# Kernel tuning notes

Measured on AMD Instinct MI355X. Metric: run time of the kernel, lower is better.

The kernel has to match this reference:

```python
import jax, jax.numpy as jnp
import numpy as np

NUM_HEADS = 12


def setup_inputs() -> dict:
    key = jax.random.key(0)
    ks = jax.random.split(key, 8)
    B, H, W, C = 1, 64, 64, 768
    hd = C // NUM_HEADS
    s = 0.02
    return {
        "hidden_states": jax.random.normal(ks[0], (B, H, W, C), jnp.float32),
        "q_w": jax.random.normal(ks[1], (C, C), jnp.float32) * s,
        "q_b": jnp.zeros((C,), jnp.float32),
        "k_w": jax.random.normal(ks[2], (C, C), jnp.float32) * s,
        "k_b": jnp.zeros((C,), jnp.float32),
        "v_w": jax.random.normal(ks[3], (C, C), jnp.float32) * s,
        "v_b": jnp.zeros((C,), jnp.float32),
        "proj_w": jax.random.normal(ks[4], (C, C), jnp.float32) * s,
        "proj_b": jnp.zeros((C,), jnp.float32),
        "rel_pos_h": jax.random.normal(ks[5], (2 * H - 1, hd), jnp.float32) * s,
        "rel_pos_w": jax.random.normal(ks[6], (2 * W - 1, hd), jnp.float32) * s,
    }


def reference(hidden_states, q_w, q_b, k_w, k_b, v_w, v_b, proj_w, proj_b,
              rel_pos_h, rel_pos_w):
    B, H, W, C = hidden_states.shape
    nh = NUM_HEADS
    hd = C // nh
    scale = hd ** -0.5

    x = hidden_states.reshape(B, H * W, C)

    def to_heads(t):  # [B, HW, C] -> [B*nh, HW, hd]
        return t.reshape(B, H * W, nh, hd).transpose(0, 2, 1, 3).reshape(B * nh, H * W, hd)

    q = to_heads(x @ q_w.T + q_b)
    k = to_heads(x @ k_w.T + k_b)
    v = to_heads(x @ v_w.T + v_b)

    # scaled QK^T: [B*nh, HW, HW]
    attn = jnp.einsum("bqd,bkd->bqk", q * scale, k)

    # decomposed relative position bias (q_size == k_size, so no interpolation)
    idx_h = jnp.arange(H)[:, None] - jnp.arange(H)[None, :] + (H - 1)
    idx_w = jnp.arange(W)[:, None] - jnp.arange(W)[None, :] + (W - 1)
    Rh = rel_pos_h[idx_h]  # [H, H, hd]
    Rw = rel_pos_w[idx_w]  # [W, W, hd]
    r_q = q.reshape(B * nh, H, W, hd)
    rel_h = jnp.einsum("bhwc,hkc->bhwk", r_q, Rh)  # [B*nh, H, W, H]
    rel_w = jnp.einsum("bhwc,wkc->bhwk", r_q, Rw)  # [B*nh, H, W, W]
    attn = (attn.reshape(B * nh, H, W, H, W)
            + rel_h[:, :, :, :, None]
            + rel_w[:, :, :, None, :]).reshape(B * nh, H * W, H * W)

    attn = jax.nn.softmax(attn.astype(jnp.float32), axis=-1).astype(q.dtype)
    # dropout p=0.0 in eval -> identity

    out = jnp.einsum("bqk,bkd->bqd", attn, v)
    out = out.reshape(B, nh, H, W, hd).transpose(0, 2, 3, 1, 4).reshape(B, H, W, C)
    out = out @ proj_w.T + proj_b
    return out
```

## Files before the change

### kernel.cpp

```cpp
#include <hip/hip_runtime.h>
#include <cstdint>
#include <cstddef>

#define T 4096
#define C 768
#define HD 64
#define NH 12

typedef float f32x4 __attribute__((ext_vector_type(4)));
typedef __bf16 bf16x8 __attribute__((ext_vector_type(8)));
typedef short s16x4 __attribute__((ext_vector_type(4)));
typedef unsigned short u16;

static __device__ __forceinline__ u16 f2bf(float f) {
    union { __bf16 h; u16 u; } cv;
    cv.h = (__bf16)f;
    return cv.u;
}

static __device__ __forceinline__ float exp2_hw(float x) {
    float r;
    asm("v_exp_f32 %0, %1" : "=v"(r) : "v"(x));
    return r;
}

static __device__ __forceinline__ void load_lds16(const void* g, void* l) {
    __builtin_amdgcn_global_load_lds(
        (const __attribute__((address_space(1))) void*)g,
        (__attribute__((address_space(3))) void*)l, 16, 0, 0);
}

static __device__ __forceinline__ void mfma16(f32x4& acc, s16x4 a, s16x4 b) {
#if defined(__HIP_DEVICE_COMPILE__)
#if __has_builtin(__builtin_amdgcn_mfma_f32_16x16x16bf16_1k)
    acc = __builtin_amdgcn_mfma_f32_16x16x16bf16_1k(a, b, acc, 0, 0, 0);
#else
    asm volatile("s_nop 2\n\t"
                 "v_mfma_f32_16x16x16_bf16 %0, %1, %2, %0\n\t"
                 "s_nop 7\n\t"
                 "s_nop 7"
                 : "+v"(acc) : "v"(a), "v"(b));
#endif
#else
    (void)acc; (void)a; (void)b;
#endif
}

__global__ __launch_bounds__(256) void cvt_main(
    const float* __restrict__ hs, const float* __restrict__ w0,
    const float* __restrict__ w1, const float* __restrict__ w2,
    const float* __restrict__ w3,
    u16* __restrict__ dhs, u16* __restrict__ dw0, u16* __restrict__ dw1,
    u16* __restrict__ dw2, u16* __restrict__ dw3) {
    const int NHS = T * C;
    const int NW = C * C;
    int i = (blockIdx.x * 256 + threadIdx.x) * 4;
    const float* s; u16* d; int j;
    if (i < NHS) { s = hs; d = dhs; j = i; }
    else {
        j = i - NHS;
        int t = j / NW; j -= t * NW;
        s = (t == 0) ? w0 : (t == 1) ? w1 : (t == 2) ? w2 : w3;
        d = (t == 0) ? dw0 : (t == 1) ? dw1 : (t == 2) ? dw2 : dw3;
    }
    float4 v = *(const float4*)(s + j);
    d[j + 0] = f2bf(v.x);
    d[j + 1] = f2bf(v.y);
    d[j + 2] = f2bf(v.z);
    d[j + 3] = f2bf(v.w);
}

__global__ __launch_bounds__(256) void cvt_rel(const float* __restrict__ rh,
                                               const float* __restrict__ rw,
                                               u16* __restrict__ drh,
                                               u16* __restrict__ drw) {
    const int N = 127 * HD;
    int i = (blockIdx.x * 256 + threadIdx.x) * 4;
    if (i >= 2 * N) return;
    const float* s = (i < N) ? rh : rw;
    u16* d = (i < N) ? drh : drw;
    int j = (i < N) ? i : i - N;
    float4 v = *(const float4*)(s + j);
    d[j + 0] = f2bf(v.x);
    d[j + 1] = f2bf(v.y);
    d[j + 2] = f2bf(v.z);
    d[j + 3] = f2bf(v.w);
}

__global__ __launch_bounds__(256, 2) void gemm_qkv_kernel(
    const u16* __restrict__ xb,
    const u16* __restrict__ wq, const u16* __restrict__ wk, const u16* __restrict__ wv,
    const float* __restrict__ qb, const float* __restrict__ kb, const float* __restrict__ vb,
    u16* __restrict__ Q, u16* __restrict__ K, u16* __restrict__ V) {
    __shared__ __align__(16) u16 As[2][128 * 64];
    __shared__ __align__(16) u16 Bs[2][128 * 64];
    const int z = blockIdx.z;
    const u16* W = (z == 0) ? wq : (z == 1) ? wk : wv;
    const float* bias = (z == 0) ? qb : (z == 1) ? kb : vb;
    u16* dst = (z == 0) ? Q : (z == 1) ? K : V;
    const int m0 = blockIdx.x * 128, n0 = blockIdx.y * 128;
    const int tid = threadIdx.x;
    const int wave = tid >> 6, lane = tid & 63, quad = lane >> 4, l15 = lane & 15;
    const int r0 = (wave >> 1) * 64, c0 = (wave & 1) * 64;
    int srow[4], sx[4], sdst[4];
#pragma unroll
    for (int i = 0; i < 4; ++i) {
        int p = i * 256 + wave * 64 + lane;
        srow[i] = p >> 3;
        sx[i] = (p & 7) ^ (srow[i] & 7);
        sdst[i] = (i * 256 + wave * 64) * 8;
    }
    f32x4 acc[4][4] = {};
#pragma unroll
    for (int i = 0; i < 4; ++i) {
        load_lds16(xb + (size_t)(m0 + srow[i]) * C + sx[i] * 8, &As[0][sdst[i]]);
        load_lds16(W + (size_t)(n0 + srow[i]) * C + sx[i] * 8, &Bs[0][sdst[i]]);
    }
    for (int kt = 0; kt < 12; ++kt) {
        const int cur = kt & 1;
        __syncthreads();
        if (kt < 11) {
            const int k0 = (kt + 1) * 64;
#pragma unroll
            for (int i = 0; i < 4; ++i) {
                load_lds16(xb + (size_t)(m0 + srow[i]) * C + k0 + sx[i] * 8, &As[cur ^ 1][sdst[i]]);
                load_lds16(W + (size_t)(n0 + srow[i]) * C + k0 + sx[i] * 8, &Bs[cur ^ 1][sdst[i]]);
            }
        }
#pragma unroll
        for (int kk = 0; kk < 2; ++kk) {
            bf16x8 af[4], bfr[4];
#pragma unroll
            for (int mi = 0; mi < 4; ++mi) {
                int r = r0 + mi * 16 + l15;
                af[mi] = *(const bf16x8*)&As[cur][r * 64 + (((kk * 4 + quad) ^ (r & 7)) * 8)];
            }
#pragma unroll
            for (int ni = 0; ni < 4; ++ni) {
                int r = c0 + ni * 16 + l15;
                bfr[ni] = *(const bf16x8*)&Bs[cur][r * 64 + (((kk * 4 + quad) ^ (r & 7)) * 8)];
            }
#pragma unroll
            for (int mi = 0; mi < 4; ++mi)
#pragma unroll
                for (int ni = 0; ni < 4; ++ni)
                    acc[mi][ni] = __builtin_amdgcn_mfma_f32_16x16x32_bf16(af[mi], bfr[ni], acc[mi][ni], 0, 0, 0);
        }
    }
#pragma unroll
    for (int mi = 0; mi < 4; ++mi)
#pragma unroll
        for (int ni = 0; ni < 4; ++ni)
#pragma unroll
            for (int r = 0; r < 4; ++r) {
                int m = m0 + r0 + mi * 16 + quad * 4 + r;
                int n = n0 + c0 + ni * 16 + l15;
                float v = acc[mi][ni][r] + bias[n];
                dst[(size_t)(n >> 6) * T * HD + (size_t)m * HD + (n & 63)] = f2bf(v);
            }
}

__global__ __launch_bounds__(256, 2) void gemm_proj_kernel(
    const u16* __restrict__ A, const u16* __restrict__ W,
    const float* __restrict__ bias, float* __restrict__ out) {
    __shared__ __align__(16) u16 As[2][128 * 64];
    __shared__ __align__(16) u16 Bs[2][128 * 64];
    const int m0 = blockIdx.x * 128, n0 = blockIdx.y * 128;
    const int tid = threadIdx.x;
    const int wave = tid >> 6, lane = tid & 63, quad = lane >> 4, l15 = lane & 15;
    const int r0 = (wave >> 1) * 64, c0 = (wave & 1) * 64;
    int srow[4], sx[4], sdst[4];
#pragma unroll
    for (int i = 0; i < 4; ++i) {
        int p = i * 256 + wave * 64 + lane;
        srow[i] = p >> 3;
        sx[i] = (p & 7) ^ (srow[i] & 7);
        sdst[i] = (i * 256 + wave * 64) * 8;
    }
    f32x4 acc[4][4] = {};
#pragma unroll
    for (int i = 0; i < 4; ++i) {
        load_lds16(A + (size_t)(m0 + srow[i]) * C + sx[i] * 8, &As[0][sdst[i]]);
        load_lds16(W + (size_t)(n0 + srow[i]) * C + sx[i] * 8, &Bs[0][sdst[i]]);
    }
    for (int kt = 0; kt < 12; ++kt) {
        const int cur = kt & 1;
        __syncthreads();
        if (kt < 11) {
            const int k0 = (kt + 1) * 64;
#pragma unroll
            for (int i = 0; i < 4; ++i) {
                load_lds16(A + (size_t)(m0 + srow[i]) * C + k0 + sx[i] * 8, &As[cur ^ 1][sdst[i]]);
                load_lds16(W + (size_t)(n0 + srow[i]) * C + k0 + sx[i] * 8, &Bs[cur ^ 1][sdst[i]]);
            }
        }
#pragma unroll
        for (int kk = 0; kk < 2; ++kk) {
            bf16x8 af[4], bfr[4];
#pragma unroll
            for (int mi = 0; mi < 4; ++mi) {
                int r = r0 + mi * 16 + l15;
                af[mi] = *(const bf16x8*)&As[cur][r * 64 + (((kk * 4 + quad) ^ (r & 7)) * 8)];
            }
#pragma unroll
            for (int ni = 0; ni < 4; ++ni) {
                int r = c0 + ni * 16 + l15;
                bfr[ni] = *(const bf16x8*)&Bs[cur][r * 64 + (((kk * 4 + quad) ^ (r & 7)) * 8)];
            }
#pragma unroll
            for (int mi = 0; mi < 4; ++mi)
#pragma unroll
                for (int ni = 0; ni < 4; ++ni)
                    acc[mi][ni] = __builtin_amdgcn_mfma_f32_16x16x32_bf16(af[mi], bfr[ni], acc[mi][ni], 0, 0, 0);
        }
    }
#pragma unroll
    for (int mi = 0; mi < 4; ++mi)
#pragma unroll
        for (int ni = 0; ni < 4; ++ni)
#pragma unroll
            for (int r = 0; r < 4; ++r) {
                int m = m0 + r0 + mi * 16 + quad * 4 + r;
                int n = n0 + c0 + ni * 16 + l15;
                out[(size_t)m * C + n] = acc[mi][ni][r] + bias[n];
            }
}

__global__ __launch_bounds__(256) void vtrans_kernel(const u16* __restrict__ V,
                                                     u16* __restrict__ Vt) {
    __shared__ __align__(16) u16 tl[64 * 72];
    const int h = blockIdx.y, t0 = blockIdx.x * 64, tid = threadIdx.x;
#pragma unroll
    for (int i = 0; i < 2; ++i) {
        int c = i * 256 + tid;
        int row = c >> 3, col = (c & 7) * 8;
        union { float4 f; u16 u[8]; } cv;
        cv.f = *(const float4*)(V + (size_t)h * T * HD + (size_t)(t0 + row) * HD + col);
#pragma unroll
        for (int j = 0; j < 8; ++j) tl[(col + j) * 72 + row] = cv.u[j];
    }
    __syncthreads();
#pragma unroll
    for (int i = 0; i < 2; ++i) {
        int c = i * 256 + tid;
        int drow = c >> 3, tcol = (c & 7) * 8;
        float4 v = *(const float4*)&tl[drow * 72 + tcol];
        *(float4*)(Vt + (size_t)(h * HD + drow) * T + t0 + tcol) = v;
    }
}

__global__ __launch_bounds__(256) void relh_kernel(const u16* __restrict__ Q,
                                                   const u16* __restrict__ rph,
                                                   float* __restrict__ relH) {
    const float LOG2E = 1.4426950408889634f;
    const int hq = blockIdx.x, h = blockIdx.y;
    const int tid = threadIdx.x, wave = tid >> 6, lane = tid & 63;
    const int quad = lane >> 4, l15 = lane & 15;
    f32x4 acc[4] = {};
    bf16x8 a[2], b[4][2];
#pragma unroll
    for (int kk = 0; kk < 2; ++kk) {
        int hk = wave * 16 + l15;
        a[kk] = *(const bf16x8*)(rph + (size_t)(hq - hk + 63) * HD + kk * 32 + quad * 8);
    }
#pragma unroll
    for (int nt = 0; nt < 4; ++nt)
#pragma unroll
        for (int kk = 0; kk < 2; ++kk)
            b[nt][kk] = *(const bf16x8*)(Q + (size_t)h * T * HD +
                                         (size_t)(hq * 64 + nt * 16 + l15) * HD + kk * 32 + quad * 8);
#pragma unroll
    for (int nt = 0; nt < 4; ++nt) {
        acc[nt] = __builtin_amdgcn_mfma_f32_16x16x32_bf16(a[0], b[nt][0], acc[nt], 0, 0, 0);
        acc[nt] = __builtin_amdgcn_mfma_f32_16x16x32_bf16(a[1], b[nt][1], acc[nt], 0, 0, 0);
    }
#pragma unroll
    for (int nt = 0; nt < 4; ++nt) {
        float4 v;
        v.x = acc[nt][0] * LOG2E; v.y = acc[nt][1] * LOG2E;
        v.z = acc[nt][2] * LOG2E; v.w = acc[nt][3] * LOG2E;
        *(float4*)(relH + (((size_t)(h * 64 + hq) * 64 + nt * 16 + l15) * 64) +
                   wave * 16 + quad * 4) = v;
    }
}

__global__ __launch_bounds__(256) void relw_kernel(const u16* __restrict__ Q,
                                                   const u16* __restrict__ rpw,
                                                   float* __restrict__ relW) {
    const float LOG2E = 1.4426950408889634f;
    const int wq = blockIdx.x, h = blockIdx.y;
    const int tid = threadIdx.x, wave = tid >> 6, lane = tid & 63;
    const int quad = lane >> 4, l15 = lane & 15;
    f32x4 acc[4] = {};
    bf16x8 a[2], b[4][2];
#pragma unroll
    for (int kk = 0; kk < 2; ++kk) {
        int hqr = wave * 16 + l15;
        a[kk] = *(const bf16x8*)(Q + (size_t)h * T * HD +
                                 (size_t)(hqr * 64 + wq) * HD + kk * 32 + quad * 8);
    }
#pragma unroll
    for (int nt = 0; nt < 4; ++nt)
#pragma unroll
        for (int kk = 0; kk < 2; ++kk) {
            int wk = nt * 16 + l15;
            b[nt][kk] = *(const bf16x8*)(rpw + (size_t)(wq - wk + 63) * HD + kk * 32 + quad * 8);
        }
#pragma unroll
    for (int nt = 0; nt < 4; ++nt) {
        acc[nt] = __builtin_amdgcn_mfma_f32_16x16x32_bf16(a[0], b[nt][0], acc[nt], 0, 0, 0);
        acc[nt] = __builtin_amdgcn_mfma_f32_16x16x32_bf16(a[1], b[nt][1], acc[nt], 0, 0, 0);
    }
#pragma unroll
    for (int nt = 0; nt < 4; ++nt)
#pragma unroll
        for (int r = 0; r < 4; ++r) {
            int hqr = wave * 16 + quad * 4 + r;
            relW[((size_t)h * T + hqr * 64 + wq) * 64 + nt * 16 + l15] = acc[nt][r] * LOG2E;
        }
}

__global__ __launch_bounds__(256, 3) void attn_kernel(
    const u16* __restrict__ Q, const u16* __restrict__ K, const u16* __restrict__ Vt,
    const float* __restrict__ relH, const float* __restrict__ relW,
    u16* __restrict__ AO) {
    __shared__ __align__(16) u16 kbuf[2][64 * 64];
    __shared__ __align__(16) u16 vbuf[2][64 * 64];
    const int hq = blockIdx.x, h = blockIdx.y;
    const int t0 = hq * 64;
    const int tid = threadIdx.x, wave = tid >> 6, lane = tid & 63;
    const int quad = lane >> 4, l15 = lane & 15;
    const float C1 = 0.18033688011112042f;

    const u16* Kbase = K + (size_t)h * T * HD;
    const u16* Vbase = Vt + (size_t)h * HD * T;

    const int p0 = wave * 128 + lane, p1 = p0 + 64;
    const int sr0 = p0 >> 3, sx0 = (p0 & 7) ^ (sr0 & 7);
    const int sr1 = p1 >> 3, sx1 = (p1 & 7) ^ (sr1 & 7);
    const int lds0 = wave * 1024, lds1 = wave * 1024 + 512;

    bf16x8 qa[2];
#pragma unroll
    for (int kk = 0; kk < 2; ++kk)
        qa[kk] = *(const bf16x8*)(Q + (size_t)h * T * HD +
                                  (size_t)(t0 + wave * 16 + l15) * HD + kk * 32 + quad * 8);
    const float* rwb = relW + ((size_t)h * T + (t0 + wave * 16 + l15)) * 64;
    float4 rw4[4];
#pragma unroll
    for (int g = 0; g < 4; ++g)
        rw4[g] = *(const float4*)(rwb + g * 16 + quad * 4);
    const float* rhb = relH + ((size_t)(h * 64 + hq) * 64 + wave * 16 + l15) * 64;

    s16x4 ones;
#pragma unroll
    for (int j = 0; j < 4; ++j) ones[j] = (short)0x3F80;

    f32x4 oa[4] = {};
    f32x4 lacc = {};

    load_lds16(Kbase + sr0 * HD + sx0 * 8, &kbuf[0][lds0]);
    load_lds16(Kbase + sr1 * HD + sx1 * 8, &kbuf[0][lds1]);
    load_lds16(Vbase + (size_t)sr0 * T + sx0 * 8, &vbuf[0][lds0]);
    load_lds16(Vbase + (size_t)sr1 * T + sx1 * 8, &vbuf[0][lds1]);

    for (int hk4 = 0; hk4 < 16; ++hk4) {
        float4 rh4 = *(const float4*)(rhb + hk4 * 4);
#pragma unroll
        for (int rr = 0; rr < 4; ++rr) {
            const int hk = hk4 * 4 + rr;
            const int cur = rr & 1;
            __syncthreads();
            if (hk < 63) {
                const int tk0 = (hk + 1) * 64;
                load_lds16(Kbase + (size_t)(tk0 + sr0) * HD + sx0 * 8, &kbuf[cur ^ 1][lds0]);
                load_lds16(Kbase + (size_t)(tk0 + sr1) * HD + sx1 * 8, &kbuf[cur ^ 1][lds1]);
                load_lds16(Vbase + (size_t)sr0 * T + tk0 + sx0 * 8, &vbuf[cur ^ 1][lds0]);
                load_lds16(Vbase + (size_t)sr1 * T + tk0 + sx1 * 8, &vbuf[cur ^ 1][lds1]);
            }
            const u16* kc = kbuf[cur];
            const u16* vc = vbuf[cur];
            f32x4 s4[4] = {};
#pragma unroll
            for (int g = 0; g < 4; ++g)
#pragma unroll
                for (int kk = 0; kk < 2; ++kk) {
                    bf16x8 af = *(const bf16x8*)&kc[g * 1024 + l15 * 64 +
                                                    (((kk * 4 + quad) ^ (l15 & 7)) * 8)];
                    s4[g] = __builtin_amdgcn_mfma_f32_16x16x32_bf16(af, qa[kk], s4[g], 0, 0, 0);
                }
            const float rhc = (rr == 0) ? rh4.x : (rr == 1) ? rh4.y : (rr == 2) ? rh4.z : rh4.w;
            s16x4 pB[4];
#pragma unroll
            for (int g = 0; g < 4; ++g) {
#pragma unroll
                for (int r = 0; r < 4; ++r) {
                    float e = exp2_hw(s4[g][r] * C1 + (rhc + rw4[g][r]));
                    pB[g][r] = (short)f2bf(e);
                }
            }
#pragma unroll
            for (int g = 0; g < 4; ++g) {
                mfma16(lacc, ones, pB[g]);
#pragma unroll
                for (int dg = 0; dg < 4; ++dg) {
                    s16x4 vf = *(const s16x4*)&vc[dg * 1024 + l15 * 64 +
                                                  (((2 * g + (quad >> 1)) ^ (l15 & 7)) * 8) +
                                                  (quad & 1) * 4];
                    mfma16(oa[dg], vf, pB[g]);
                }
            }
        }
    }
    const float inv = 1.0f / lacc[0];
    const size_t trow = (size_t)(t0 + wave * 16 + l15) * C + h * HD;
#pragma unroll
    for (int dg = 0; dg < 4; ++dg) {
        unsigned int lo = (unsigned int)f2bf(oa[dg][0] * inv) |
                          ((unsigned int)f2bf(oa[dg][1] * inv) << 16);
        unsigned int hi = (unsigned int)f2bf(oa[dg][2] * inv) |
                          ((unsigned int)f2bf(oa[dg][3] * inv) << 16);
        uint2 st; st.x = lo; st.y = hi;
        *(uint2*)(AO + trow + dg * 16 + quad * 4) = st;
    }
}

extern "C" void kernel_launch(void* const* d_in, const int* in_sizes, int n_in,
                              void* d_out, int out_size, void* d_ws, size_t ws_size,
                              hipStream_t stream) {
    (void)in_sizes; (void)n_in; (void)out_size; (void)ws_size;
    const float* hs  = (const float*)d_in[0];
    const float* q_w = (const float*)d_in[1];
    const float* q_b = (const float*)d_in[2];
    const float* k_w = (const float*)d_in[3];
    const float* k_b = (const float*)d_in[4];
    const float* v_w = (const float*)d_in[5];
    const float* v_b = (const float*)d_in[6];
    const float* p_w = (const float*)d_in[7];
    const float* p_b = (const float*)d_in[8];
    const float* rph = (const float*)d_in[9];
    const float* rpw = (const float*)d_in[10];

    char* ws = (char*)d_ws;
    size_t off = 0;
    auto alloc = [&](size_t bytes) {
        void* p = ws + off;
        off = (off + bytes + 255) & ~(size_t)255;
        return p;
    };
    u16* xb   = (u16*)alloc((size_t)T * C * 2);
    u16* wqb  = (u16*)alloc((size_t)C * C * 2);
    u16* wkb  = (u16*)alloc((size_t)C * C * 2);
    u16* wvb  = (u16*)alloc((size_t)C * C * 2);
    u16* wpb  = (u16*)alloc((size_t)C * C * 2);
    u16* rphb = (u16*)alloc((size_t)127 * HD * 2);
    u16* rpwb = (u16*)alloc((size_t)127 * HD * 2);
    u16* Qb   = (u16*)alloc((size_t)NH * T * HD * 2);
    u16* Kb   = (u16*)alloc((size_t)NH * T * HD * 2);
    u16* Vb   = (u16*)alloc((size_t)NH * T * HD * 2);
    u16* Vt   = (u16*)alloc((size_t)NH * T * HD * 2);
    float* relH = (float*)alloc((size_t)NH * T * 64 * 4);
    float* relW = (float*)alloc((size_t)NH * T * 64 * 4);
    u16* AO   = (u16*)alloc((size_t)T * C * 2);

    const int nmain = (T * C + 4 * C * C) / 4 / 256;
    cvt_main<<<dim3(nmain), dim3(256), 0, stream>>>(hs, q_w, k_w, v_w, p_w,
                                                    xb, wqb, wkb, wvb, wpb);
    cvt_rel<<<dim3(16), dim3(256), 0, stream>>>(rph, rpw, rphb, rpwb);

    gemm_qkv_kernel<<<dim3(32, 6, 3), dim3(256), 0, stream>>>(
        xb, wqb, wkb, wvb, q_b, k_b, v_b, Qb, Kb, Vb);
    vtrans_kernel<<<dim3(64, NH), dim3(256), 0, stream>>>(Vb, Vt);
    relh_kernel<<<dim3(64, NH), dim3(256), 0, stream>>>(Qb, rphb, relH);
    relw_kernel<<<dim3(64, NH), dim3(256), 0, stream>>>(Qb, rpwb, relW);
    attn_kernel<<<dim3(64, NH), dim3(256), 0, stream>>>(Qb, Kb, Vt, relH, relW, AO);
    gemm_proj_kernel<<<dim3(32, 6), dim3(256), 0, stream>>>(AO, wpb, p_b, (float*)d_out);
}
```

Measured before the change: 241.7 us.

## Split attention key tile across waves, fuse cvt kernels, drop ones-MFMA row sum

Each wave in the attention kernel now handles a 16-key slice of every 64-key tile for all four query bands, instead of all keys for one 16-query band. This cuts the per-wave LDS reads of K and V fragments and reuses them across bands. Partial outputs and row sums are reduced across waves through shared memory at the end. The row sum is now computed with VALU adds instead of an extra MFMA against a ones vector. The two conversion kernels are merged into one launch. In exchange, per-thread accumulators grow fourfold (oa[4][4], qa[4][2]), which raises register pressure and may lower occupancy, and the final cross-wave reduction adds LDS traffic and barriers.

```diff
diff --git a/kernel.cpp b/kernel.cpp
--- a/kernel.cpp
+++ b/kernel.cpp
@@ -46,40 +46,32 @@
 #endif
 }
 
-__global__ __launch_bounds__(256) void cvt_main(
+__global__ __launch_bounds__(256) void cvt_all(
     const float* __restrict__ hs, const float* __restrict__ w0,
     const float* __restrict__ w1, const float* __restrict__ w2,
-    const float* __restrict__ w3,
+    const float* __restrict__ w3, const float* __restrict__ rh,
+    const float* __restrict__ rw,
     u16* __restrict__ dhs, u16* __restrict__ dw0, u16* __restrict__ dw1,
-    u16* __restrict__ dw2, u16* __restrict__ dw3) {
+    u16* __restrict__ dw2, u16* __restrict__ dw3, u16* __restrict__ drh,
+    u16* __restrict__ drw) {
     const int NHS = T * C;
     const int NW = C * C;
+    const int NR = 127 * HD;
+    const int NTOT = NHS + 4 * NW + 2 * NR;
     int i = (blockIdx.x * 256 + threadIdx.x) * 4;
+    if (i >= NTOT) return;
     const float* s; u16* d; int j;
     if (i < NHS) { s = hs; d = dhs; j = i; }
-    else {
+    else if (i < NHS + 4 * NW) {
         j = i - NHS;
         int t = j / NW; j -= t * NW;
         s = (t == 0) ? w0 : (t == 1) ? w1 : (t == 2) ? w2 : w3;
         d = (t == 0) ? dw0 : (t == 1) ? dw1 : (t == 2) ? dw2 : dw3;
-    }
-    float4 v = *(const float4*)(s + j);
-    d[j + 0] = f2bf(v.x);
-    d[j + 1] = f2bf(v.y);
-    d[j + 2] = f2bf(v.z);
-    d[j + 3] = f2bf(v.w);
-}
-
-__global__ __launch_bounds__(256) void cvt_rel(const float* __restrict__ rh,
-                                               const float* __restrict__ rw,
-                                               u16* __restrict__ drh,
-                                               u16* __restrict__ drw) {
-    const int N = 127 * HD;
-    int i = (blockIdx.x * 256 + threadIdx.x) * 4;
-    if (i >= 2 * N) return;
-    const float* s = (i < N) ? rh : rw;
-    u16* d = (i < N) ? drh : drw;
-    int j = (i < N) ? i : i - N;
+    } else {
+        j = i - NHS - 4 * NW;
+        if (j < NR) { s = rh; d = drh; }
+        else { s = rw; d = drw; j -= NR; }
+    }
     float4 v = *(const float4*)(s + j);
     d[j + 0] = f2bf(v.x);
     d[j + 1] = f2bf(v.y);
@@ -324,48 +316,53 @@
     const u16* __restrict__ Q, const u16* __restrict__ K, const u16* __restrict__ Vt,
     const float* __restrict__ relH, const float* __restrict__ relW,
     u16* __restrict__ AO) {
-    __shared__ __align__(16) u16 kbuf[2][64 * 64];
-    __shared__ __align__(16) u16 vbuf[2][64 * 64];
+    __shared__ __align__(16) unsigned char smem[46080];
+    u16* kb = (u16*)smem;
+    u16* vb = (u16*)(smem + 16384);
+    float* fs = (float*)smem;
+    float* rs = (float*)(smem + 45056);
+
     const int hq = blockIdx.x, h = blockIdx.y;
     const int t0 = hq * 64;
-    const int tid = threadIdx.x, wave = tid >> 6, lane = tid & 63;
+    const int tid = threadIdx.x, w = tid >> 6, lane = tid & 63;
     const int quad = lane >> 4, l15 = lane & 15;
     const float C1 = 0.18033688011112042f;
 
     const u16* Kbase = K + (size_t)h * T * HD;
     const u16* Vbase = Vt + (size_t)h * HD * T;
 
-    const int p0 = wave * 128 + lane, p1 = p0 + 64;
+    const int p0 = w * 128 + lane, p1 = p0 + 64;
     const int sr0 = p0 >> 3, sx0 = (p0 & 7) ^ (sr0 & 7);
     const int sr1 = p1 >> 3, sx1 = (p1 & 7) ^ (sr1 & 7);
-    const int lds0 = wave * 1024, lds1 = wave * 1024 + 512;
-
-    bf16x8 qa[2];
-#pragma unroll
-    for (int kk = 0; kk < 2; ++kk)
-        qa[kk] = *(const bf16x8*)(Q + (size_t)h * T * HD +
-                                  (size_t)(t0 + wave * 16 + l15) * HD + kk * 32 + quad * 8);
-    const float* rwb = relW + ((size_t)h * T + (t0 + wave * 16 + l15)) * 64;
-    float4 rw4[4];
-#pragma unroll
-    for (int g = 0; g < 4; ++g)
-        rw4[g] = *(const float4*)(rwb + g * 16 + quad * 4);
-    const float* rhb = relH + ((size_t)(h * 64 + hq) * 64 + wave * 16 + l15) * 64;
-
-    s16x4 ones;
-#pragma unroll
-    for (int j = 0; j < 4; ++j) ones[j] = (short)0x3F80;
-
-    f32x4 oa[4] = {};
-    f32x4 lacc = {};
-
-    load_lds16(Kbase + sr0 * HD + sx0 * 8, &kbuf[0][lds0]);
-    load_lds16(Kbase + sr1 * HD + sx1 * 8, &kbuf[0][lds1]);
-    load_lds16(Vbase + (size_t)sr0 * T + sx0 * 8, &vbuf[0][lds0]);
-    load_lds16(Vbase + (size_t)sr1 * T + sx1 * 8, &vbuf[0][lds1]);
+    const int lds0 = w * 1024, lds1 = w * 1024 + 512;
+
+    bf16x8 qa[4][2];
+#pragma unroll
+    for (int band = 0; band < 4; ++band)
+#pragma unroll
+        for (int kk = 0; kk < 2; ++kk)
+            qa[band][kk] = *(const bf16x8*)(Q + (size_t)h * T * HD +
+                                            (size_t)(t0 + band * 16 + l15) * HD + kk * 32 + quad * 8);
+    f32x4 rw4[4];
+#pragma unroll
+    for (int band = 0; band < 4; ++band)
+        rw4[band] = *(const f32x4*)(relW + ((size_t)h * T + t0 + band * 16 + l15) * 64 +
+                                    w * 16 + quad * 4);
+    const float* rhB = relH + ((size_t)(h * 64 + hq) * 64 + l15) * 64;
+
+    f32x4 oa[4][4] = {};
+    float lsum[4] = {0.f, 0.f, 0.f, 0.f};
+
+    load_lds16(Kbase + sr0 * HD + sx0 * 8, &kb[lds0]);
+    load_lds16(Kbase + sr1 * HD + sx1 * 8, &kb[lds1]);
+    load_lds16(Vbase + (size_t)sr0 * T + sx0 * 8, &vb[lds0]);
+    load_lds16(Vbase + (size_t)sr1 * T + sx1 * 8, &vb[lds1]);
 
     for (int hk4 = 0; hk4 < 16; ++hk4) {
-        float4 rh4 = *(const float4*)(rhb + hk4 * 4);
+        f32x4 rh4[4];
+#pragma unroll
+        for (int band = 0; band < 4; ++band)
+            rh4[band] = *(const f32x4*)(rhB + band * 1024 + hk4 * 4);
 #pragma unroll
         for (int rr = 0; rr < 4; ++rr) {
             const int hk = hk4 * 4 + rr;
@@ -373,55 +370,77 @@
             __syncthreads();
             if (hk < 63) {
                 const int tk0 = (hk + 1) * 64;
-                load_lds16(Kbase + (size_t)(tk0 + sr0) * HD + sx0 * 8, &kbuf[cur ^ 1][lds0]);
-                load_lds16(Kbase + (size_t)(tk0 + sr1) * HD + sx1 * 8, &kbuf[cur ^ 1][lds1]);
-                load_lds16(Vbase + (size_t)sr0 * T + tk0 + sx0 * 8, &vbuf[cur ^ 1][lds0]);
-                load_lds16(Vbase + (size_t)sr1 * T + tk0 + sx1 * 8, &vbuf[cur ^ 1][lds1]);
-            }
-            const u16* kc = kbuf[cur];
-            const u16* vc = vbuf[cur];
-            f32x4 s4[4] = {};
-#pragma unroll
-            for (int g = 0; g < 4; ++g)
-#pragma unroll
-                for (int kk = 0; kk < 2; ++kk) {
-                    bf16x8 af = *(const bf16x8*)&kc[g * 1024 + l15 * 64 +
-                                                    (((kk * 4 + quad) ^ (l15 & 7)) * 8)];
-                    s4[g] = __builtin_amdgcn_mfma_f32_16x16x32_bf16(af, qa[kk], s4[g], 0, 0, 0);
-                }
-            const float rhc = (rr == 0) ? rh4.x : (rr == 1) ? rh4.y : (rr == 2) ? rh4.z : rh4.w;
-            s16x4 pB[4];
-#pragma unroll
-            for (int g = 0; g < 4; ++g) {
-#pragma unroll
-                for (int r = 0; r < 4; ++r) {
-                    float e = exp2_hw(s4[g][r] * C1 + (rhc + rw4[g][r]));
-                    pB[g][r] = (short)f2bf(e);
-                }
-            }
-#pragma unroll
-            for (int g = 0; g < 4; ++g) {
-                mfma16(lacc, ones, pB[g]);
-#pragma unroll
-                for (int dg = 0; dg < 4; ++dg) {
-                    s16x4 vf = *(const s16x4*)&vc[dg * 1024 + l15 * 64 +
-                                                  (((2 * g + (quad >> 1)) ^ (l15 & 7)) * 8) +
-                                                  (quad & 1) * 4];
-                    mfma16(oa[dg], vf, pB[g]);
-                }
-            }
-        }
-    }
-    const float inv = 1.0f / lacc[0];
-    const size_t trow = (size_t)(t0 + wave * 16 + l15) * C + h * HD;
-#pragma unroll
-    for (int dg = 0; dg < 4; ++dg) {
-        unsigned int lo = (unsigned int)f2bf(oa[dg][0] * inv) |
-                          ((unsigned int)f2bf(oa[dg][1] * inv) << 16);
-        unsigned int hi = (unsigned int)f2bf(oa[dg][2] * inv) |
-                          ((unsigned int)f2bf(oa[dg][3] * inv) << 16);
-        uint2 st; st.x = lo; st.y = hi;
-        *(uint2*)(AO + trow + dg * 16 + quad * 4) = st;
+                load_lds16(Kbase + (size_t)(tk0 + sr0) * HD + sx0 * 8, &kb[(cur ^ 1) * 4096 + lds0]);
+                load_lds16(Kbase + (size_t)(tk0 + sr1) * HD + sx1 * 8, &kb[(cur ^ 1) * 4096 + lds1]);
+                load_lds16(Vbase + (size_t)sr0 * T + tk0 + sx0 * 8, &vb[(cur ^ 1) * 4096 + lds0]);
+                load_lds16(Vbase + (size_t)sr1 * T + tk0 + sx1 * 8, &vb[(cur ^ 1) * 4096 + lds1]);
+            }
+            const u16* kc = kb + cur * 4096;
+            const u16* vc = vb + cur * 4096;
+            bf16x8 af0 = *(const bf16x8*)&kc[(w * 16 + l15) * 64 + ((quad ^ (l15 & 7)) * 8)];
+            bf16x8 af1 = *(const bf16x8*)&kc[(w * 16 + l15) * 64 + (((4 + quad) ^ (l15 & 7)) * 8)];
+            s16x4 vf[4];
+#pragma unroll
+            for (int dg = 0; dg < 4; ++dg)
+                vf[dg] = *(const s16x4*)&vc[(dg * 16 + l15) * 64 +
+                                            (((w * 2 + (quad >> 1)) ^ (l15 & 7)) * 8) +
+                                            (quad & 1) * 4];
+#pragma unroll
+            for (int band = 0; band < 4; ++band) {
+                f32x4 s4 = {};
+                s4 = __builtin_amdgcn_mfma_f32_16x16x32_bf16(af0, qa[band][0], s4, 0, 0, 0);
+                s4 = __builtin_amdgcn_mfma_f32_16x16x32_bf16(af1, qa[band][1], s4, 0, 0, 0);
+                const float rhc = rh4[band][rr];
+                float e0 = exp2_hw(s4[0] * C1 + rhc + rw4[band][0]);
+                float e1 = exp2_hw(s4[1] * C1 + rhc + rw4[band][1]);
+                float e2 = exp2_hw(s4[2] * C1 + rhc + rw4[band][2]);
+                float e3 = exp2_hw(s4[3] * C1 + rhc + rw4[band][3]);
+                lsum[band] += (e0 + e1) + (e2 + e3);
+                s16x4 pB;
+                pB[0] = (short)f2bf(e0); pB[1] = (short)f2bf(e1);
+                pB[2] = (short)f2bf(e2); pB[3] = (short)f2bf(e3);
+#pragma unroll
+                for (int dg = 0; dg < 4; ++dg)
+                    mfma16(oa[band][dg], vf[dg], pB);
+            }
+        }
+    }
+    __syncthreads();
+#pragma unroll
+    for (int band = 0; band < 4; ++band) {
+        float t = lsum[band];
+        t += __shfl_xor(t, 16);
+        t += __shfl_xor(t, 32);
+        if (quad == 0) rs[w * 64 + band * 16 + l15] = t;
+    }
+    __syncthreads();
+    const int qe = w * 16 + l15;
+    const float inv = 1.0f / (rs[qe] + rs[64 + qe] + rs[128 + qe] + rs[192 + qe]);
+#pragma unroll
+    for (int half = 0; half < 2; ++half) {
+#pragma unroll
+        for (int band = 0; band < 4; ++band)
+#pragma unroll
+            for (int dgl = 0; dgl < 2; ++dgl)
+                *(f32x4*)&fs[(size_t)(w * 64 + band * 16 + l15) * 44 + dgl * 16 + quad * 4] =
+                    oa[band][half * 2 + dgl];
+        __syncthreads();
+        float o[8] = {};
+#pragma unroll
+        for (int p = 0; p < 4; ++p)
+#pragma unroll
+            for (int j = 0; j < 2; ++j) {
+                f32x4 t4 = *(const f32x4*)&fs[(size_t)(p * 64 + qe) * 44 + quad * 8 + j * 4];
+                o[j * 4 + 0] += t4[0]; o[j * 4 + 1] += t4[1];
+                o[j * 4 + 2] += t4[2]; o[j * 4 + 3] += t4[3];
+            }
+        uint4 st;
+        st.x = (unsigned)f2bf(o[0] * inv) | ((unsigned)f2bf(o[1] * inv) << 16);
+        st.y = (unsigned)f2bf(o[2] * inv) | ((unsigned)f2bf(o[3] * inv) << 16);
+        st.z = (unsigned)f2bf(o[4] * inv) | ((unsigned)f2bf(o[5] * inv) << 16);
+        st.w = (unsigned)f2bf(o[6] * inv) | ((unsigned)f2bf(o[7] * inv) << 16);
+        *(uint4*)(AO + (size_t)(t0 + qe) * C + h * 64 + half * 32 + quad * 8) = st;
+        __syncthreads();
     }
 }
 
@@ -463,10 +482,9 @@
     float* relW = (float*)alloc((size_t)NH * T * 64 * 4);
     u16* AO   = (u16*)alloc((size_t)T * C * 2);
 
-    const int nmain = (T * C + 4 * C * C) / 4 / 256;
-    cvt_main<<<dim3(nmain), dim3(256), 0, stream>>>(hs, q_w, k_w, v_w, p_w,
-                                                    xb, wqb, wkb, wvb, wpb);
-    cvt_rel<<<dim3(16), dim3(256), 0, stream>>>(rph, rpw, rphb, rpwb);
+    const int NTOT = T * C + 4 * C * C + 2 * 127 * HD;
+    cvt_all<<<dim3((NTOT / 4 + 255) / 256), dim3(256), 0, stream>>>(
+        hs, q_w, k_w, v_w, p_w, rph, rpw, xb, wqb, wkb, wvb, wpb, rphb, rpwb);
 
     gemm_qkv_kernel<<<dim3(32, 6, 3), dim3(256), 0, stream>>>(
         xb, wqb, wkb, wvb, q_b, k_b, v_b, Qb, Kb, Vb);
```

Result: slower. 518.0 us (+114.4%).
